# Performance work log

Measured on AMD Instinct MI355X. Metric: run time of the kernel, lower is better.

## Reference

```python
import jax, jax.numpy as jnp
import numpy as np

B, S, L, D, H, DH, DFF, V = 16, 512, 12, 512, 8, 64, 2048, 631
MAX_KLEN = 1024  # tgt_len + mem_len


def _ln(x, g, b, eps=1e-5):
    m = x.mean(-1, keepdims=True)
    v = ((x - m) ** 2).mean(-1, keepdims=True)
    return (x - m) / jnp.sqrt(v + eps) * g + b


def _rot_half(x):
    # interleaved pair rotation: (x0,x1,x2,x3,..) -> (-x1,x0,-x3,x2,..)
    xe = x[..., ::2]
    xo = x[..., 1::2]
    return jnp.stack((-xo, xe), axis=-1).reshape(x.shape)


def _sin_cos(seq_len, d_head):
    inv_freq = 1.0 / 10000.0 ** (jnp.arange(0, d_head, 2, dtype=jnp.float32) / d_head)
    t = jnp.arange(seq_len, dtype=jnp.float32)[:, None] * inv_freq[None, :]
    sin = jnp.repeat(jnp.sin(t), 2, axis=-1)  # (S, DH)
    cos = jnp.repeat(jnp.cos(t), 2, axis=-1)
    return sin, cos


def setup_inputs() -> dict:
    key = jax.random.key(0)
    ks = jax.random.split(key, 12)
    std = 0.02
    data = jax.random.randint(ks[0], (B, S), 0, V)
    emb = jax.random.normal(ks[1], (V, D), jnp.float32) * std
    pos = jax.random.normal(ks[2], (MAX_KLEN, D), jnp.float32) * std
    Wq = jax.random.normal(ks[3], (L, D, H * DH), jnp.float32) * std
    Wkv = jax.random.normal(ks[4], (L, D, 2 * H * DH), jnp.float32) * std
    Wo = jax.random.normal(ks[5], (L, H * DH, D), jnp.float32) * std
    W1 = jax.random.normal(ks[6], (L, D, DFF), jnp.float32) * std
    b1 = jnp.zeros((L, DFF), jnp.float32)
    W2 = jax.random.normal(ks[7], (L, DFF, D), jnp.float32) * std
    b2 = jnp.zeros((L, D), jnp.float32)
    ln1_g = jnp.ones((L, D), jnp.float32)
    ln1_b = jnp.zeros((L, D), jnp.float32)
    ln2_g = jnp.ones((L, D), jnp.float32)
    ln2_b = jnp.zeros((L, D), jnp.float32)
    out_b = jnp.zeros((V,), jnp.float32)
    return dict(data=data, emb=emb, pos=pos, Wq=Wq, Wkv=Wkv, Wo=Wo,
                W1=W1, b1=b1, W2=W2, b2=b2,
                ln1_g=ln1_g, ln1_b=ln1_b, ln2_g=ln2_g, ln2_b=ln2_b, out_b=out_b)


def reference(data, emb, pos, Wq, Wkv, Wo, W1, b1, W2, b2,
              ln1_g, ln1_b, ln2_g, ln2_b, out_b):
    sin, cos = _sin_cos(S, DH)
    sin = sin[None, :, None, :]  # (1,S,1,DH) broadcast over (B,S,H,DH)
    cos = cos[None, :, None, :]
    causal = jnp.triu(jnp.ones((S, S), bool), 1)
    scale = 1.0 / jnp.sqrt(jnp.float32(DH))

    h = emb[data] + pos[:S][None]  # (B,S,D)
    for l in range(L):
        q = (h @ Wq[l]).reshape(B, S, H, DH)
        kv = h @ Wkv[l]
        k = kv[..., :H * DH].reshape(B, S, H, DH)
        v = kv[..., H * DH:].reshape(B, S, H, DH)
        q = q * cos + _rot_half(q) * sin
        k = k * cos + _rot_half(k) * sin
        sc = jnp.einsum('bqhd,bkhd->bhqk', q, k) * scale
        sc = jnp.where(causal[None, None], -jnp.inf, sc)
        p = jax.nn.softmax(sc, axis=-1)
        av = jnp.einsum('bhqk,bkhd->bqhd', p, v).reshape(B, S, H * DH)
        h = _ln(h + av @ Wo[l], ln1_g[l], ln1_b[l])
        ff = jax.nn.relu(h @ W1[l] + b1[l]) @ W2[l] + b2[l]
        h = _ln(h + ff, ln2_g[l], ln2_b[l])
    # tied output projection: out_layer.weight = word_emb.weight, plus bias
    return h @ emb.T + out_b
```

## Files before the change

kernel.cpp:

```cpp
#include <hip/hip_runtime.h>
#include <hip/hip_bf16.h>

typedef __hip_bfloat16 bf16;
typedef __attribute__((ext_vector_type(8))) short short8;
typedef __attribute__((ext_vector_type(4))) float f32x4;

static constexpr int Bz = 16, Sq = 512, Lw = 12, Dm = 512, Hh = 8, DFFd = 2048, Vv = 631;
static constexpr int Mtok = Bz * Sq;
static constexpr int VPAD = 640;
static constexpr int QKS = 1024;

__device__ __forceinline__ bf16 f2b(float x) { return __float2bfloat16(x); }
__device__ __forceinline__ float bfu(unsigned short s) {
    union { unsigned u; float f; } c; c.u = (unsigned)s << 16; return c.f;
}

__device__ __forceinline__ f32x4 z4() { f32x4 v; v[0]=0.f; v[1]=0.f; v[2]=0.f; v[3]=0.f; return v; }

__device__ __forceinline__ void gload_lds16(const bf16* g, bf16* l) {
    __builtin_amdgcn_global_load_lds(
        (const __attribute__((address_space(1))) unsigned int*)(g),
        (__attribute__((address_space(3))) unsigned int*)(l),
        16, 0, 0);
}

__global__ void k_sincos(float* __restrict__ cosT, float* __restrict__ sinT) {
    int i = blockIdx.x * 256 + threadIdx.x;
    int s = i >> 5, f = i & 31;
    float inv = powf(10000.0f, -(float)(2 * f) / 64.0f);
    float t = (float)s * inv;
    sinT[i] = sinf(t);
    cosT[i] = cosf(t);
}

__global__ void k_embconv(const float* __restrict__ emb, bf16* __restrict__ embT) {
    int i = blockIdx.x * 256 + threadIdx.x;
    int n = i >> 9;
    embT[i] = (n < Vv) ? f2b(emb[i]) : f2b(0.0f);
}

__global__ void k_embed(const int* __restrict__ data, const float* __restrict__ emb,
                        const float* __restrict__ pos, float* __restrict__ hf, bf16* __restrict__ hb) {
    int tok = blockIdx.x;
    int id = data[tok];
    int s = tok & (Sq - 1);
    for (int d = threadIdx.x; d < Dm; d += 256) {
        float v = emb[id * Dm + d] + pos[s * Dm + d];
        hf[(size_t)tok * Dm + d] = v;
        hb[(size_t)tok * Dm + d] = f2b(v);
    }
}

__global__ void k_wtrans(const float* __restrict__ src, bf16* __restrict__ dst,
                         int K, int N, long long sStride, long long dStride) {
    src += (long long)blockIdx.z * sStride;
    dst += (long long)blockIdx.z * dStride;
    __shared__ float tile[32][33];
    int k0 = blockIdx.y * 32, n0 = blockIdx.x * 32;
    int tx = threadIdx.x & 31, ty = threadIdx.x >> 5;
    #pragma unroll
    for (int r = ty; r < 32; r += 8) tile[r][tx] = src[(size_t)(k0 + r) * N + n0 + tx];
    __syncthreads();
    #pragma unroll
    for (int r = ty; r < 32; r += 8) dst[(size_t)(n0 + r) * K + k0 + tx] = f2b(tile[tx][r]);
}

template<int EPI>
__global__ __launch_bounds__(512) void k_gemmW(const bf16* __restrict__ A, const bf16* __restrict__ Bt,
                                               void* __restrict__ Cout, void* __restrict__ Cout2,
                                               const float* __restrict__ bias,
                                               const float* __restrict__ cosT, const float* __restrict__ sinT,
                                               int M, int N, int K, int ldA, int ldB) {
    extern __shared__ __align__(16) char smem[];
    bf16* lAbase = (bf16*)smem;
    bf16* lBbase = (bf16*)(smem + 3 * 256 * 32 * 2);

    const int t = threadIdx.x;
    const int lane = t & 63;
    const int wave = t >> 6;
    const int wr = wave >> 1, wc = wave & 1;
    const int l15 = lane & 15, l4 = lane >> 4;

    const int gx = gridDim.x, gy = gridDim.y;
    const int nwg = gx * gy * gridDim.z;
    const int cpx = nwg >> 3;
    int lin = (blockIdx.z * gy + blockIdx.y) * gx + blockIdx.x;
    lin = (lin & 7) * cpx + (lin >> 3);
    const int bn = lin % gx;
    const int rem = lin / gx;
    const int bm = rem % gy;
    const int bz = rem / gy;

    const bf16* Ab = A + (size_t)(bm * 256) * ldA + (size_t)bz * K;
    const bf16* Bb = Bt + (size_t)(bn * 128) * ldB + (size_t)bz * K;

    int soffA[2], soffB0;
    #pragma unroll
    for (int p = 0; p < 2; p++) {
        int q = p * 512 + t, r = q >> 2, s = q & 3;
        soffA[p] = r * ldA + ((s ^ ((r >> 1) & 3)) << 3);
    }
    {
        int r = t >> 2, s = t & 3;
        soffB0 = r * ldB + ((s ^ ((r >> 1) & 3)) << 3);
    }

    f32x4 acc[4][4];
    #pragma unroll
    for (int i = 0; i < 4; i++)
        #pragma unroll
        for (int j = 0; j < 4; j++) acc[i][j] = z4();

    auto STAGE = [&](int buf, int kt) {
        const int k0 = kt << 5;
        bf16* la = lAbase + buf * (256 * 32);
        bf16* lb = lBbase + buf * (128 * 32);
        #pragma unroll
        for (int p = 0; p < 2; p++)
            gload_lds16(Ab + (size_t)soffA[p] + k0, &la[(p * 512 + t) * 8]);
        gload_lds16(Bb + (size_t)soffB0 + k0, &lb[t * 8]);
    };

    auto COMPUTE = [&](int buf) {
        const char* la = (const char*)(lAbase + buf * (256 * 32));
        const char* lb = (const char*)(lBbase + buf * (128 * 32));
        short8 af[4], bfr[4];
        #pragma unroll
        for (int i = 0; i < 4; i++) {
            int row = wr * 64 + i * 16 + l15;
            af[i] = *(const short8*)(la + row * 64 + (((l4 ^ (row >> 1)) & 3) << 4));
        }
        #pragma unroll
        for (int j = 0; j < 4; j++) {
            int row = wc * 64 + j * 16 + l15;
            bfr[j] = *(const short8*)(lb + row * 64 + (((l4 ^ (row >> 1)) & 3) << 4));
        }
        #pragma unroll
        for (int i = 0; i < 4; i++)
            #pragma unroll
            for (int j = 0; j < 4; j++)
                acc[i][j] = __builtin_amdgcn_mfma_f32_16x16x32_bf16(af[i], bfr[j], acc[i][j], 0, 0, 0);
    };

    const int nk = K >> 5;
    STAGE(0, 0);
    STAGE(1, 1);
    int kt = 0;
    for (; kt < nk - 1; ++kt) {
        asm volatile("s_waitcnt vmcnt(3)" ::: "memory");
        __builtin_amdgcn_s_barrier();
        if (kt + 2 < nk) STAGE((kt + 2) % 3, kt + 2);
        __builtin_amdgcn_s_setprio(1);
        COMPUTE(kt % 3);
        __builtin_amdgcn_s_setprio(0);
    }
    asm volatile("s_waitcnt vmcnt(0)" ::: "memory");
    __builtin_amdgcn_s_barrier();
    __builtin_amdgcn_s_setprio(1);
    COMPUTE(kt % 3);
    __builtin_amdgcn_s_setprio(0);

    #pragma unroll
    for (int i = 0; i < 4; i++) {
        #pragma unroll
        for (int j = 0; j < 4; j++) {
            const int col = bn * 128 + wc * 64 + j * 16 + l15;
            const int row0 = bm * 256 + wr * 64 + i * 16 + l4 * 4;
            if (EPI == 4 && col >= 1024) {
                int h = (col - 1024) >> 6, d = (col - 1024) & 63;
                int b = row0 >> 9, s0 = row0 & 511;
                bf16 pk[4];
                #pragma unroll
                for (int r = 0; r < 4; r++) pk[r] = f2b(acc[i][j][r]);
                *(ushort4*)&((bf16*)Cout2)[((size_t)(b * 8 + h) * 64 + d) * 512 + s0] =
                    *(const ushort4*)pk;
                continue;
            }
            #pragma unroll
            for (int r = 0; r < 4; r++) {
                int row = row0 + r;
                float v = acc[i][j][r];
                if (EPI == 1) {
                    bf16* Co = (bf16*)(bz ? Cout2 : Cout);
                    Co[(size_t)row * N + col] = f2b(v);
                } else if (EPI == 2) {
                    v += bias[col];
                    v = v > 0.f ? v : 0.f;
                    ((bf16*)Cout)[(size_t)row * N + col] = f2b(v);
                } else if (EPI == 3) {
                    if (col < Vv) ((float*)Cout)[(size_t)row * Vv + col] = v + bias[col];
                } else {
                    float p = __shfl_xor(v, 1, 64);
                    int srow = row & (Sq - 1);
                    int f = (col >> 1) & 31;
                    float cc = cosT[srow * 32 + f], sn = sinT[srow * 32 + f];
                    float o = (col & 1) ? (v * cc + p * sn) : (v * cc - p * sn);
                    if (col < 512) o *= 0.125f;
                    ((bf16*)Cout)[(size_t)row * QKS + col] = f2b(o);
                }
            }
        }
    }
}

__global__ __launch_bounds__(512) void k_attn(const bf16* __restrict__ qkv,
                                              const bf16* __restrict__ vt, bf16* __restrict__ av) {
    __shared__ __align__(16) bf16 lK[64][80];
    __shared__ __align__(16) bf16 lV[64][80];
    __shared__ __align__(16) bf16 lP[8][16][80];
    const int tq = blockIdx.x, bh = blockIdx.y;
    const int b = bh >> 3, h = bh & 7;
    const int t = threadIdx.x, lane = t & 63, w = t >> 6;
    const int l15 = lane & 15, l4 = lane >> 4;
    const int q0 = tq * 128;
    const int rowb = q0 + w * 16;

    short8 qf[2];
    {
        const bf16* qr = qkv + (size_t)(b * Sq + rowb + l15) * QKS + h * 64 + l4 * 8;
        qf[0] = *(const short8*)qr;
        qf[1] = *(const short8*)(qr + 32);
    }
    f32x4 o[4];
    #pragma unroll
    for (int j = 0; j < 4; j++) o[j] = z4();
    float mrow[4] = {-1e30f, -1e30f, -1e30f, -1e30f};
    float ssum[4] = {0.f, 0.f, 0.f, 0.f};

    const int nk = (q0 >> 6) + 2;
    for (int kt = 0; kt < nk; ++kt) {
        int kv0 = kt * 64;
        __syncthreads();
        {
            int r = t >> 3, c = (t & 7) * 8;
            *(uint4*)&lK[r][c] = *(const uint4*)&qkv[(size_t)(b * Sq + kv0 + r) * QKS + 512 + h * 64 + c];
            *(uint4*)&lV[r][c] = *(const uint4*)&vt[(size_t)(bh * 64 + r) * 512 + kv0 + c];
        }
        __syncthreads();

        f32x4 sc[4];
        #pragma unroll
        for (int j = 0; j < 4; j++) sc[j] = z4();
        #pragma unroll
        for (int j = 0; j < 4; j++)
            #pragma unroll
            for (int ks = 0; ks < 2; ks++) {
                short8 kf = *(const short8*)&lK[j * 16 + l15][ks * 32 + l4 * 8];
                sc[j] = __builtin_amdgcn_mfma_f32_16x16x32_bf16(qf[ks], kf, sc[j], 0, 0, 0);
            }
        if (kv0 + 63 > rowb) {
            #pragma unroll
            for (int j = 0; j < 4; j++)
                #pragma unroll
                for (int r = 0; r < 4; r++)
                    if (kv0 + j * 16 + l15 > rowb + l4 * 4 + r) sc[j][r] = -1e30f;
        }
        float corr[4];
        #pragma unroll
        for (int r = 0; r < 4; r++) {
            float m_ = fmaxf(fmaxf(sc[0][r], sc[1][r]), fmaxf(sc[2][r], sc[3][r]));
            #pragma unroll
            for (int d = 1; d < 16; d <<= 1) m_ = fmaxf(m_, __shfl_xor(m_, d, 64));
            float mo = mrow[r];
            float mn = fmaxf(mo, m_);
            mrow[r] = mn;
            corr[r] = __expf(mo - mn);
        }
        float p[4][4];
        #pragma unroll
        for (int j = 0; j < 4; j++)
            #pragma unroll
            for (int r = 0; r < 4; r++)
                p[j][r] = __expf(sc[j][r] - mrow[r]);
        #pragma unroll
        for (int r = 0; r < 4; r++)
            ssum[r] = ssum[r] * corr[r] + p[0][r] + p[1][r] + p[2][r] + p[3][r];
        #pragma unroll
        for (int j = 0; j < 4; j++)
            #pragma unroll
            for (int r = 0; r < 4; r++)
                lP[w][l4 * 4 + r][j * 16 + l15] = f2b(p[j][r]);
        #pragma unroll
        for (int j = 0; j < 4; j++) {
            o[j][0] *= corr[0]; o[j][1] *= corr[1]; o[j][2] *= corr[2]; o[j][3] *= corr[3];
        }
        #pragma unroll
        for (int ks = 0; ks < 2; ks++) {
            short8 pa = *(const short8*)&lP[w][l15][ks * 32 + l4 * 8];
            #pragma unroll
            for (int j = 0; j < 4; j++) {
                short8 vb = *(const short8*)&lV[j * 16 + l15][ks * 32 + l4 * 8];
                o[j] = __builtin_amdgcn_mfma_f32_16x16x32_bf16(pa, vb, o[j], 0, 0, 0);
            }
        }
    }
    #pragma unroll
    for (int r = 0; r < 4; r++) {
        float s = ssum[r];
        #pragma unroll
        for (int d = 1; d < 16; d <<= 1) s += __shfl_xor(s, d, 64);
        ssum[r] = 1.f / s;
    }
    #pragma unroll
    for (int j = 0; j < 4; j++)
        #pragma unroll
        for (int r = 0; r < 4; r++)
            av[(size_t)(b * Sq + rowb + l4 * 4 + r) * 512 + h * 64 + j * 16 + l15] = f2b(o[j][r] * ssum[r]);
}

template<bool ADDB>
__global__ __launch_bounds__(256) void k_addln(float* __restrict__ hf, bf16* __restrict__ hb,
                                               const bf16* __restrict__ d1, const bf16* __restrict__ d2,
                                               const float* __restrict__ bias,
                                               const float* __restrict__ gamma, const float* __restrict__ beta) {
    const int lane = threadIdx.x & 63, w = threadIdx.x >> 6;
    const int row = blockIdx.x * 4 + w;
    const size_t base = (size_t)row * Dm + lane * 8;
    float v[8];
    float4 h0 = *(const float4*)&hf[base];
    float4 h1 = *(const float4*)&hf[base + 4];
    short8 a8 = *(const short8*)&d1[base];
    short8 b8 = *(const short8*)&d2[base];
    v[0] = h0.x; v[1] = h0.y; v[2] = h0.z; v[3] = h0.w;
    v[4] = h1.x; v[5] = h1.y; v[6] = h1.z; v[7] = h1.w;
    #pragma unroll
    for (int k = 0; k < 8; k++)
        v[k] += bfu((unsigned short)a8[k]) + bfu((unsigned short)b8[k]);
    if (ADDB) {
        float4 bb0 = *(const float4*)&bias[lane * 8];
        float4 bb1 = *(const float4*)&bias[lane * 8 + 4];
        v[0] += bb0.x; v[1] += bb0.y; v[2] += bb0.z; v[3] += bb0.w;
        v[4] += bb1.x; v[5] += bb1.y; v[6] += bb1.z; v[7] += bb1.w;
    }
    float s = 0.f, sq = 0.f;
    #pragma unroll
    for (int k = 0; k < 8; k++) { s += v[k]; sq += v[k] * v[k]; }
    #pragma unroll
    for (int m = 1; m < 64; m <<= 1) { s += __shfl_xor(s, m, 64); sq += __shfl_xor(sq, m, 64); }
    float mean = s * (1.f / Dm);
    float var = sq * (1.f / Dm) - mean * mean;
    float inv = rsqrtf(var + 1e-5f);
    float4 g0 = *(const float4*)&gamma[lane * 8];
    float4 g1 = *(const float4*)&gamma[lane * 8 + 4];
    float4 e0 = *(const float4*)&beta[lane * 8];
    float4 e1 = *(const float4*)&beta[lane * 8 + 4];
    float gs[8] = {g0.x, g0.y, g0.z, g0.w, g1.x, g1.y, g1.z, g1.w};
    float es[8] = {e0.x, e0.y, e0.z, e0.w, e1.x, e1.y, e1.z, e1.w};
    float ov[8];
    short8 ob;
    #pragma unroll
    for (int k = 0; k < 8; k++) {
        ov[k] = (v[k] - mean) * inv * gs[k] + es[k];
        ob[k] = (short)__bfloat16_as_ushort(f2b(ov[k]));
    }
    float4 o0; o0.x = ov[0]; o0.y = ov[1]; o0.z = ov[2]; o0.w = ov[3];
    float4 o1; o1.x = ov[4]; o1.y = ov[5]; o1.z = ov[6]; o1.w = ov[7];
    *(float4*)&hf[base] = o0;
    *(float4*)&hf[base + 4] = o1;
    *(short8*)&hb[base] = ob;
}

extern "C" void kernel_launch(void* const* d_in, const int* in_sizes, int n_in,
                              void* d_out, int out_size, void* d_ws, size_t ws_size,
                              hipStream_t stream) {
    const int*   data = (const int*)d_in[0];
    const float* emb  = (const float*)d_in[1];
    const float* pos  = (const float*)d_in[2];
    const float* Wq   = (const float*)d_in[3];
    const float* Wkv  = (const float*)d_in[4];
    const float* Wo   = (const float*)d_in[5];
    const float* W1   = (const float*)d_in[6];
    const float* b1   = (const float*)d_in[7];
    const float* W2   = (const float*)d_in[8];
    const float* b2   = (const float*)d_in[9];
    const float* ln1g = (const float*)d_in[10];
    const float* ln1b = (const float*)d_in[11];
    const float* ln2g = (const float*)d_in[12];
    const float* ln2b = (const float*)d_in[13];
    const float* outb = (const float*)d_in[14];
    float* out = (float*)d_out;
    char* ws = (char*)d_ws;

    const int WLDS = 3 * (256 * 32 + 128 * 32) * 2;
    (void)hipFuncSetAttribute((const void*)&k_gemmW<1>, hipFuncAttributeMaxDynamicSharedMemorySize, WLDS);
    (void)hipFuncSetAttribute((const void*)&k_gemmW<2>, hipFuncAttributeMaxDynamicSharedMemorySize, WLDS);
    (void)hipFuncSetAttribute((const void*)&k_gemmW<3>, hipFuncAttributeMaxDynamicSharedMemorySize, WLDS);
    (void)hipFuncSetAttribute((const void*)&k_gemmW<4>, hipFuncAttributeMaxDynamicSharedMemorySize, WLDS);

    size_t off = 0;
    auto take = [&](size_t bytes) { size_t r = off; off += (bytes + 255) & ~(size_t)255; return r; };
    float* hf    = (float*)(ws + take((size_t)Mtok * Dm * 4));
    bf16*  hb    = (bf16*)(ws + take((size_t)Mtok * Dm * 2));
    bf16*  qkvbf = (bf16*)(ws + take((size_t)Mtok * QKS * 2));
    bf16*  vtb   = (bf16*)(ws + take((size_t)Mtok * Dm * 2));
    bf16*  avb   = (bf16*)(ws + take((size_t)Mtok * Dm * 2));
    bf16*  tmpb  = (bf16*)(ws + take((size_t)Mtok * Dm * 2));
    bf16*  tmp2b = (bf16*)(ws + take((size_t)Mtok * Dm * 2));
    bf16*  ff1   = (bf16*)(ws + take((size_t)Mtok * DFFd * 2));
    float* cosT  = (float*)(ws + take((size_t)Sq * 32 * 4));
    float* sinT  = (float*)(ws + take((size_t)Sq * 32 * 4));
    bf16*  embT  = (bf16*)(ws + take((size_t)VPAD * Dm * 2));

    const size_t ofsQKV = 0;
    const size_t ofsO   = ofsQKV + (size_t)1536 * 512;
    const size_t ofsW1  = ofsO + (size_t)512 * 512;
    const size_t ofsW2  = ofsW1 + (size_t)512 * 2048;
    const size_t SLABE  = ofsW2 + (size_t)2048 * 512;

    bf16* wT = (bf16*)(ws + off);
    size_t remain = (ws_size > off) ? (ws_size - off) : 0;
    bool upfront = remain >= SLABE * 12 * 2;

    k_sincos<<<(Sq * 32) / 256, 256, 0, stream>>>(cosT, sinT);
    k_embconv<<<(VPAD * Dm) / 256, 256, 0, stream>>>(emb, embT);
    k_embed<<<Mtok, 256, 0, stream>>>(data, emb, pos, hf, hb);

    if (upfront) {
        k_wtrans<<<dim3(16, 16, 12), 256, 0, stream>>>(Wq,  wT + ofsQKV,             512, 512,  (long long)512 * 512,  (long long)SLABE);
        k_wtrans<<<dim3(32, 16, 12), 256, 0, stream>>>(Wkv, wT + ofsQKV + 512 * 512, 512, 1024, (long long)512 * 1024, (long long)SLABE);
        k_wtrans<<<dim3(16, 16, 12), 256, 0, stream>>>(Wo,  wT + ofsO,  512, 512,  (long long)512 * 512,  (long long)SLABE);
        k_wtrans<<<dim3(64, 16, 12), 256, 0, stream>>>(W1,  wT + ofsW1, 512, 2048, (long long)512 * 2048, (long long)SLABE);
        k_wtrans<<<dim3(16, 64, 12), 256, 0, stream>>>(W2,  wT + ofsW2, 2048, 512, (long long)2048 * 512, (long long)SLABE);
    }

    for (int l = 0; l < Lw; l++) {
        bf16* slab = wT + (upfront ? (size_t)l * SLABE : 0);
        if (!upfront) {
            k_wtrans<<<dim3(16, 16, 1), 256, 0, stream>>>(Wq  + (size_t)l * 512 * 512,  slab + ofsQKV,             512, 512,  0, 0);
            k_wtrans<<<dim3(32, 16, 1), 256, 0, stream>>>(Wkv + (size_t)l * 512 * 1024, slab + ofsQKV + 512 * 512, 512, 1024, 0, 0);
            k_wtrans<<<dim3(16, 16, 1), 256, 0, stream>>>(Wo  + (size_t)l * 512 * 512,  slab + ofsO,  512, 512,  0, 0);
            k_wtrans<<<dim3(64, 16, 1), 256, 0, stream>>>(W1  + (size_t)l * 512 * 2048, slab + ofsW1, 512, 2048, 0, 0);
            k_wtrans<<<dim3(16, 64, 1), 256, 0, stream>>>(W2  + (size_t)l * 2048 * 512, slab + ofsW2, 2048, 512, 0, 0);
        }
        k_gemmW<4><<<dim3(12, 32, 1), 512, WLDS, stream>>>(hb, slab + ofsQKV, qkvbf, vtb, nullptr, cosT, sinT,
                                                           Mtok, 1536, 512, 512, 512);
        k_attn<<<dim3(4, 128), 512, 0, stream>>>(qkvbf, vtb, avb);
        k_gemmW<1><<<dim3(4, 32, 2), 512, WLDS, stream>>>(avb, slab + ofsO, tmpb, tmp2b, nullptr, nullptr, nullptr,
                                                          Mtok, 512, 256, 512, 512);
        k_addln<false><<<Mtok / 4, 256, 0, stream>>>(hf, hb, tmpb, tmp2b, nullptr,
                                                     ln1g + (size_t)l * Dm, ln1b + (size_t)l * Dm);
        k_gemmW<2><<<dim3(16, 32, 1), 512, WLDS, stream>>>(hb, slab + ofsW1, ff1, nullptr, b1 + (size_t)l * DFFd,
                                                           nullptr, nullptr, Mtok, 2048, 512, 512, 512);
        k_gemmW<1><<<dim3(4, 32, 2), 512, WLDS, stream>>>(ff1, slab + ofsW2, tmpb, tmp2b, nullptr, nullptr, nullptr,
                                                          Mtok, 512, 1024, 2048, 2048);
        k_addln<true><<<Mtok / 4, 256, 0, stream>>>(hf, hb, tmpb, tmp2b, b2 + (size_t)l * Dm,
                                                    ln2g + (size_t)l * Dm, ln2b + (size_t)l * Dm);
    }
    k_gemmW<3><<<dim3(5, 32, 1), 512, WLDS, stream>>>(hb, embT, out, nullptr, outb, nullptr, nullptr,
                                                      Mtok, VPAD, 512, 512, 512);
}
```

Before: 1.661 ms.

## Double-buffer K/V tiles in attention with register prefetch and causal tile skip

Result: no change. 1.647 ms (-0.8%).

```diff
diff --git a/kernel.cpp b/kernel.cpp
--- a/kernel.cpp
+++ b/kernel.cpp
@@ -205,9 +205,9 @@
 
 __global__ __launch_bounds__(512) void k_attn(const bf16* __restrict__ qkv,
                                               const bf16* __restrict__ vt, bf16* __restrict__ av) {
-    __shared__ __align__(16) bf16 lK[64][80];
-    __shared__ __align__(16) bf16 lV[64][80];
-    __shared__ __align__(16) bf16 lP[8][16][80];
+    __shared__ __align__(16) bf16 lK[2][64][80];
+    __shared__ __align__(16) bf16 lV[2][64][80];
+    __shared__ __align__(16) bf16 lP[8][16][88];
     const int tq = blockIdx.x, bh = blockIdx.y;
     const int b = bh >> 3, h = bh & 7;
     const int t = threadIdx.x, lane = t & 63, w = t >> 6;
@@ -228,71 +228,84 @@
     float ssum[4] = {0.f, 0.f, 0.f, 0.f};
 
     const int nk = (q0 >> 6) + 2;
+    const int sr = t >> 3, scc = (t & 7) * 8;
+    const bf16* gK = qkv + (size_t)(b * Sq + sr) * QKS + 512 + h * 64 + scc;
+    const bf16* gV = vt + (size_t)(bh * 64 + sr) * 512 + scc;
+    uint4 rK = *(const uint4*)gK;
+    uint4 rV = *(const uint4*)gV;
+
     for (int kt = 0; kt < nk; ++kt) {
-        int kv0 = kt * 64;
-        __syncthreads();
-        {
-            int r = t >> 3, c = (t & 7) * 8;
-            *(uint4*)&lK[r][c] = *(const uint4*)&qkv[(size_t)(b * Sq + kv0 + r) * QKS + 512 + h * 64 + c];
-            *(uint4*)&lV[r][c] = *(const uint4*)&vt[(size_t)(bh * 64 + r) * 512 + kv0 + c];
-        }
-        __syncthreads();
-
-        f32x4 sc[4];
-        #pragma unroll
-        for (int j = 0; j < 4; j++) sc[j] = z4();
-        #pragma unroll
-        for (int j = 0; j < 4; j++)
+        const int buf = kt & 1;
+        const int kv0 = kt * 64;
+        uint4 nK, nV;
+        if (kt + 1 < nk) {
+            nK = *(const uint4*)(gK + (size_t)(kt + 1) * 64 * QKS);
+            nV = *(const uint4*)(gV + (size_t)(kt + 1) * 64);
+        }
+        *(uint4*)&lK[buf][sr][scc] = rK;
+        *(uint4*)&lV[buf][sr][scc] = rV;
+        asm volatile("s_waitcnt lgkmcnt(0)" ::: "memory");
+        __builtin_amdgcn_s_barrier();
+        __builtin_amdgcn_sched_barrier(0);
+
+        if (kv0 <= rowb + 15) {
+            f32x4 sc[4];
+            #pragma unroll
+            for (int j = 0; j < 4; j++) sc[j] = z4();
+            #pragma unroll
+            for (int j = 0; j < 4; j++)
+                #pragma unroll
+                for (int ks = 0; ks < 2; ks++) {
+                    short8 kf = *(const short8*)&lK[buf][j * 16 + l15][ks * 32 + l4 * 8];
+                    sc[j] = __builtin_amdgcn_mfma_f32_16x16x32_bf16(qf[ks], kf, sc[j], 0, 0, 0);
+                }
+            if (kv0 + 63 > rowb) {
+                #pragma unroll
+                for (int j = 0; j < 4; j++)
+                    #pragma unroll
+                    for (int r = 0; r < 4; r++)
+                        if (kv0 + j * 16 + l15 > rowb + l4 * 4 + r) sc[j][r] = -1e30f;
+            }
+            float corr[4];
+            #pragma unroll
+            for (int r = 0; r < 4; r++) {
+                float m_ = fmaxf(fmaxf(sc[0][r], sc[1][r]), fmaxf(sc[2][r], sc[3][r]));
+                #pragma unroll
+                for (int d = 1; d < 16; d <<= 1) m_ = fmaxf(m_, __shfl_xor(m_, d, 64));
+                float mo = mrow[r];
+                float mn = fmaxf(mo, m_);
+                mrow[r] = mn;
+                corr[r] = __expf(mo - mn);
+            }
+            float p[4][4];
+            #pragma unroll
+            for (int j = 0; j < 4; j++)
+                #pragma unroll
+                for (int r = 0; r < 4; r++)
+                    p[j][r] = __expf(sc[j][r] - mrow[r]);
+            #pragma unroll
+            for (int r = 0; r < 4; r++)
+                ssum[r] = ssum[r] * corr[r] + p[0][r] + p[1][r] + p[2][r] + p[3][r];
+            #pragma unroll
+            for (int j = 0; j < 4; j++)
+                #pragma unroll
+                for (int r = 0; r < 4; r++)
+                    lP[w][l4 * 4 + r][j * 16 + l15] = f2b(p[j][r]);
+            #pragma unroll
+            for (int j = 0; j < 4; j++) {
+                o[j][0] *= corr[0]; o[j][1] *= corr[1]; o[j][2] *= corr[2]; o[j][3] *= corr[3];
+            }
             #pragma unroll
             for (int ks = 0; ks < 2; ks++) {
-                short8 kf = *(const short8*)&lK[j * 16 + l15][ks * 32 + l4 * 8];
-                sc[j] = __builtin_amdgcn_mfma_f32_16x16x32_bf16(qf[ks], kf, sc[j], 0, 0, 0);
-            }
-        if (kv0 + 63 > rowb) {
-            #pragma unroll
-            for (int j = 0; j < 4; j++)
-                #pragma unroll
-                for (int r = 0; r < 4; r++)
-                    if (kv0 + j * 16 + l15 > rowb + l4 * 4 + r) sc[j][r] = -1e30f;
-        }
-        float corr[4];
-        #pragma unroll
-        for (int r = 0; r < 4; r++) {
-            float m_ = fmaxf(fmaxf(sc[0][r], sc[1][r]), fmaxf(sc[2][r], sc[3][r]));
-            #pragma unroll
-            for (int d = 1; d < 16; d <<= 1) m_ = fmaxf(m_, __shfl_xor(m_, d, 64));
-            float mo = mrow[r];
-            float mn = fmaxf(mo, m_);
-            mrow[r] = mn;
-            corr[r] = __expf(mo - mn);
-        }
-        float p[4][4];
-        #pragma unroll
-        for (int j = 0; j < 4; j++)
-            #pragma unroll
-            for (int r = 0; r < 4; r++)
-                p[j][r] = __expf(sc[j][r] - mrow[r]);
-        #pragma unroll
-        for (int r = 0; r < 4; r++)
-            ssum[r] = ssum[r] * corr[r] + p[0][r] + p[1][r] + p[2][r] + p[3][r];
-        #pragma unroll
-        for (int j = 0; j < 4; j++)
-            #pragma unroll
-            for (int r = 0; r < 4; r++)
-                lP[w][l4 * 4 + r][j * 16 + l15] = f2b(p[j][r]);
-        #pragma unroll
-        for (int j = 0; j < 4; j++) {
-            o[j][0] *= corr[0]; o[j][1] *= corr[1]; o[j][2] *= corr[2]; o[j][3] *= corr[3];
-        }
-        #pragma unroll
-        for (int ks = 0; ks < 2; ks++) {
-            short8 pa = *(const short8*)&lP[w][l15][ks * 32 + l4 * 8];
-            #pragma unroll
-            for (int j = 0; j < 4; j++) {
-                short8 vb = *(const short8*)&lV[j * 16 + l15][ks * 32 + l4 * 8];
-                o[j] = __builtin_amdgcn_mfma_f32_16x16x32_bf16(pa, vb, o[j], 0, 0, 0);
-            }
-        }
+                short8 pa = *(const short8*)&lP[w][l15][ks * 32 + l4 * 8];
+                #pragma unroll
+                for (int j = 0; j < 4; j++) {
+                    short8 vb = *(const short8*)&lV[buf][j * 16 + l15][ks * 32 + l4 * 8];
+                    o[j] = __builtin_amdgcn_mfma_f32_16x16x32_bf16(pa, vb, o[j], 0, 0, 0);
+                }
+            }
+        }
+        rK = nK; rV = nV;
     }
     #pragma unroll
     for (int r = 0; r < 4; r++) {
```
